# Kernel tuning notes

Measured on AMD Instinct MI355X. Metric: run time of the kernel, lower is better.

The kernel has to match this reference:

```python
import jax, jax.numpy as jnp
import numpy as np

EMBED_DIM = 256
NUM_HEADS = 8
HEAD_DIM = EMBED_DIM // NUM_HEADS
ADJ_CHANNELS = 4
B, N = 8, 1024


def setup_inputs() -> dict:
    key = jax.random.key(0)
    ks = jax.random.split(key, 12)
    s = 1.0 / np.sqrt(EMBED_DIM)
    sa = 1.0 / np.sqrt(ADJ_CHANNELS)
    return {
        "x": jax.random.normal(ks[0], (B, N, EMBED_DIM), dtype=jnp.float32),
        "adj": jax.random.uniform(ks[1], (B, N, N, ADJ_CHANNELS), dtype=jnp.float32),
        "Wq": jax.random.uniform(ks[2], (EMBED_DIM, EMBED_DIM), jnp.float32, -s, s),
        "bq": jnp.zeros((EMBED_DIM,), jnp.float32),
        "Wk": jax.random.uniform(ks[3], (EMBED_DIM, EMBED_DIM), jnp.float32, -s, s),
        "bk": jnp.zeros((EMBED_DIM,), jnp.float32),
        "Wv": jax.random.uniform(ks[4], (EMBED_DIM, EMBED_DIM), jnp.float32, -s, s),
        "bv": jnp.zeros((EMBED_DIM,), jnp.float32),
        "Wo": jax.random.uniform(ks[5], (EMBED_DIM, EMBED_DIM), jnp.float32, -s, s),
        "bo": jnp.zeros((EMBED_DIM,), jnp.float32),
        "Wa": jax.random.uniform(ks[6], (ADJ_CHANNELS, NUM_HEADS), jnp.float32, -sa, sa),
        "ba": jnp.zeros((NUM_HEADS,), jnp.float32),
    }


def reference(x, adj, Wq, bq, Wk, bk, Wv, bv, Wo, bo, Wa, ba):
    Bs, Ns, E = x.shape
    H, D = NUM_HEADS, HEAD_DIM
    def heads(W, b):
        return (x @ W + b).reshape(Bs, Ns, H, D).transpose(0, 2, 1, 3)  # [B,H,N,D]
    Q, K, V = heads(Wq, bq), heads(Wk, bk), heads(Wv, bv)
    # adjacency-derived additive bias: [B,N,N,C] -> [B,N,N,H] -> [B,H,N,N]
    bias = jnp.moveaxis(adj @ Wa + ba, -1, 1)
    scores = jnp.einsum("bhnd,bhmd->bhnm", Q, K) / np.sqrt(D) + bias
    attn = jax.nn.softmax(scores, axis=-1)
    ctx = jnp.einsum("bhnm,bhmd->bhnd", attn, V)  # [B,H,N,D]
    ctx = ctx.transpose(0, 2, 1, 3).reshape(Bs, Ns, E)
    return ctx @ Wo + bo + x
```

## Files before the change

kernel.cpp:

```cpp
#include <hip/hip_runtime.h>
#include <hip/hip_bf16.h>

#define BATCH 8
#define SEQ   1024
#define EMB   256
#define NH    8
#define HD    32
#define QSCALE 0.2550030053f

typedef __attribute__((ext_vector_type(8))) short short8;
typedef __attribute__((ext_vector_type(4))) float floatx4;

__device__ __forceinline__ ushort f2bf(float f) {
    __hip_bfloat16 h = __float2bfloat16(f);
    return *reinterpret_cast<ushort*>(&h);
}

__device__ __forceinline__ float bf2f(ushort u) {
    unsigned v = ((unsigned)u) << 16;
    return __builtin_bit_cast(float, v);
}

__device__ __forceinline__ void gload_lds16(const float4* g, float4* l) {
    __builtin_amdgcn_global_load_lds(
        (const __attribute__((address_space(1))) unsigned int*)g,
        (__attribute__((address_space(3))) unsigned int*)l, 16, 0, 0);
}

__global__ __launch_bounds__(256) void prep_kernel(
    const float* __restrict__ Wq, const float* __restrict__ Wk,
    const float* __restrict__ Wv, const float* __restrict__ Wo,
    ushort* __restrict__ Wqt, ushort* __restrict__ Wkt,
    ushort* __restrict__ Wvt, ushort* __restrict__ Wot)
{
    __shared__ float tilebuf[32][33];
    const int blk = blockIdx.x;
    const int mat = blk >> 6, tile = blk & 63;
    const int ti = tile >> 3, tj = tile & 7;
    const float* W = (mat == 0) ? Wq : (mat == 1) ? Wk : (mat == 2) ? Wv : Wo;
    ushort* Wt = (mat == 0) ? Wqt : (mat == 1) ? Wkt : (mat == 2) ? Wvt : Wot;
    const float scale = (mat == 0) ? QSCALE : 1.0f;

    const int tx = threadIdx.x & 31, ty = threadIdx.x >> 5;
    #pragma unroll
    for (int p = 0; p < 4; ++p)
        tilebuf[ty + p * 8][tx] = W[(size_t)(ti * 32 + ty + p * 8) * EMB + tj * 32 + tx];
    __syncthreads();
    #pragma unroll
    for (int p = 0; p < 4; ++p)
        Wt[(size_t)(tj * 32 + ty + p * 8) * EMB + ti * 32 + tx] =
            f2bf(tilebuf[tx][ty + p * 8] * scale);
}

__global__ __launch_bounds__(256) void qkv_gemm(
    const float* __restrict__ x,
    const ushort* __restrict__ Wqt, const ushort* __restrict__ Wkt,
    const ushort* __restrict__ Wvt,
    const float* __restrict__ bq, const float* __restrict__ bk,
    const float* __restrict__ bv,
    ushort* __restrict__ Qb, ushort* __restrict__ Kb, ushort* __restrict__ Vt)
{
    const int mat = blockIdx.y;
    const ushort* __restrict__ Wt = (mat == 0) ? Wqt : (mat == 1) ? Wkt : Wvt;
    const float* __restrict__ bias = (mat == 0) ? bq : (mat == 1) ? bk : bv;
    const float bscale = (mat == 0) ? QSCALE : 1.0f;

    const int w = threadIdx.x >> 6, lane = threadIdx.x & 63;
    const int quad = lane >> 4, l16 = lane & 15;
    const int row0 = blockIdx.x * 64 + w * 16;

    floatx4 acc[16];
    #pragma unroll
    for (int i = 0; i < 16; ++i) acc[i] = (floatx4){0.f, 0.f, 0.f, 0.f};

    const float* __restrict__ xrow = x + (size_t)(row0 + l16) * EMB + quad * 8;

    #pragma unroll
    for (int ks = 0; ks < 8; ++ks) {
        const float4 xa0 = *(const float4*)(xrow + ks * 32);
        const float4 xa1 = *(const float4*)(xrow + ks * 32 + 4);
        ushort au[8] = {f2bf(xa0.x), f2bf(xa0.y), f2bf(xa0.z), f2bf(xa0.w),
                        f2bf(xa1.x), f2bf(xa1.y), f2bf(xa1.z), f2bf(xa1.w)};
        const short8 a = *(const short8*)au;
        #pragma unroll
        for (int i = 0; i < 16; ++i) {
            const short8 bf = *(const short8*)(Wt + (size_t)(i * 16 + l16) * EMB + ks * 32 + quad * 8);
            acc[i] = __builtin_amdgcn_mfma_f32_16x16x32_bf16(a, bf, acc[i], 0, 0, 0);
        }
    }

    const int gr0 = row0 + quad * 4;
    if (mat < 2) {
        ushort* __restrict__ dst = (mat == 0) ? Qb : Kb;
        #pragma unroll
        for (int i = 0; i < 16; ++i) {
            const int c = i * 16 + l16, h = c >> 5, d = c & (HD - 1);
            const float bb = bias[c] * bscale;
            #pragma unroll
            for (int r = 0; r < 4; ++r) {
                const int gr = gr0 + r, b = gr >> 10, n = gr & (SEQ - 1);
                dst[((size_t)(b * NH + h) * SEQ + n) * HD + d] = f2bf(acc[i][r] + bb);
            }
        }
    } else {
        const int b = gr0 >> 10, n0 = gr0 & (SEQ - 1);
        const int j0 = n0 & 31;
        const int slot = (j0 < 16) ? ((j0 >> 2) << 3)
                                   : ((((j0 - 16) >> 2) << 3) + 4);
        const int nperm = (n0 & ~31) | slot;
        #pragma unroll
        for (int i = 0; i < 16; ++i) {
            const int c = i * 16 + l16, h = c >> 5, d = c & (HD - 1);
            const float bb = bias[c];
            ushort4 t4;
            t4.x = f2bf(acc[i][0] + bb); t4.y = f2bf(acc[i][1] + bb);
            t4.z = f2bf(acc[i][2] + bb); t4.w = f2bf(acc[i][3] + bb);
            *(ushort4*)(Vt + ((size_t)(b * NH + h) * HD + d) * SEQ + nperm) = t4;
        }
    }
}

__global__ __launch_bounds__(512) void attn_kernel(
    const ushort* __restrict__ Qb, const ushort* __restrict__ Kb,
    const ushort* __restrict__ Vt, const float* __restrict__ adj,
    const float* __restrict__ Wa, const float* __restrict__ ba,
    ushort* __restrict__ cp, float* __restrict__ lsum)
{
    __shared__ float4 Atile[2][16][65];
    const int tid = threadIdx.x, h = tid >> 6, lane = tid & 63;
    const int quad = lane >> 4, l16 = lane & 15;
    const int q0 = blockIdx.x * 16, b = blockIdx.y, z = blockIdx.z;
    const int bh = b * NH + h;
    const int kz = z * 512;

    const float LOG2E = 1.4426950408889634f;
    const float wa0 = Wa[0 * NH + h] * LOG2E, wa1 = Wa[1 * NH + h] * LOG2E;
    const float wa2 = Wa[2 * NH + h] * LOG2E, wa3 = Wa[3 * NH + h] * LOG2E;
    const float bah = ba[h] * LOG2E;

    const short8 aq = *(const short8*)(Qb + ((size_t)bh * SEQ + q0 + l16) * HD + quad * 8);

    floatx4 o0 = {0.f, 0.f, 0.f, 0.f}, o1 = {0.f, 0.f, 0.f, 0.f};
    float lacc = 0.f;

    const float4* __restrict__ adjb = (const float4*)adj + (size_t)b * SEQ * SEQ;
    const float4* __restrict__ asrc0 = adjb + (size_t)(q0 + 2 * h)     * SEQ + kz + lane;
    const float4* __restrict__ asrc1 = adjb + (size_t)(q0 + 2 * h + 1) * SEQ + kz + lane;

    const ushort* __restrict__ Kbase = Kb + (size_t)bh * SEQ * HD + (size_t)l16 * HD + quad * 8;
    const ushort* __restrict__ Vb0 = Vt + ((size_t)bh * HD + l16) * SEQ + quad * 8;
    const ushort* __restrict__ Vb1 = Vt + ((size_t)bh * HD + 16 + l16) * SEQ + quad * 8;

    gload_lds16(asrc0, &Atile[0][2 * h][0]);
    gload_lds16(asrc1, &Atile[0][2 * h + 1][0]);
    __syncthreads();

    for (int it = 0; it < 8; ++it) {
        const int cur = it & 1;
        const int key0 = kz + it * 64;

        if (it < 7) {
            gload_lds16(asrc0 + (it + 1) * 64, &Atile[cur ^ 1][2 * h][0]);
            gload_lds16(asrc1 + (it + 1) * 64, &Atile[cur ^ 1][2 * h + 1][0]);
        }

        const short8 k0 = *(const short8*)(Kbase + (size_t)(key0)      * HD);
        const short8 k1 = *(const short8*)(Kbase + (size_t)(key0 + 16) * HD);
        const short8 k2 = *(const short8*)(Kbase + (size_t)(key0 + 32) * HD);
        const short8 k3 = *(const short8*)(Kbase + (size_t)(key0 + 48) * HD);
        const floatx4 zz = {0.f, 0.f, 0.f, 0.f};
        floatx4 s0 = __builtin_amdgcn_mfma_f32_16x16x32_bf16(k0, aq, zz, 0, 0, 0);
        floatx4 s1 = __builtin_amdgcn_mfma_f32_16x16x32_bf16(k1, aq, zz, 0, 0, 0);
        floatx4 s2 = __builtin_amdgcn_mfma_f32_16x16x32_bf16(k2, aq, zz, 0, 0, 0);
        floatx4 s3 = __builtin_amdgcn_mfma_f32_16x16x32_bf16(k3, aq, zz, 0, 0, 0);

        ushort pu0[8], pu1[8];
        #pragma unroll
        for (int r = 0; r < 4; ++r) {
            const int col = 4 * quad + r;
            const float4 a0 = Atile[cur][l16][col];
            const float4 a1 = Atile[cur][l16][16 + col];
            const float4 a2 = Atile[cur][l16][32 + col];
            const float4 a3 = Atile[cur][l16][48 + col];
            const float b0 = fmaf(a0.x, wa0, fmaf(a0.y, wa1, fmaf(a0.z, wa2, fmaf(a0.w, wa3, bah))));
            const float b1 = fmaf(a1.x, wa0, fmaf(a1.y, wa1, fmaf(a1.z, wa2, fmaf(a1.w, wa3, bah))));
            const float b2 = fmaf(a2.x, wa0, fmaf(a2.y, wa1, fmaf(a2.z, wa2, fmaf(a2.w, wa3, bah))));
            const float b3 = fmaf(a3.x, wa0, fmaf(a3.y, wa1, fmaf(a3.z, wa2, fmaf(a3.w, wa3, bah))));
            const float p0 = __builtin_amdgcn_exp2f(s0[r] + b0);
            const float p1 = __builtin_amdgcn_exp2f(s1[r] + b1);
            const float p2 = __builtin_amdgcn_exp2f(s2[r] + b2);
            const float p3 = __builtin_amdgcn_exp2f(s3[r] + b3);
            lacc += (p0 + p1) + (p2 + p3);
            pu0[r]     = f2bf(p0);
            pu0[4 + r] = f2bf(p1);
            pu1[r]     = f2bf(p2);
            pu1[4 + r] = f2bf(p3);
        }
        const short8 pf0 = *(const short8*)pu0;
        const short8 pf1 = *(const short8*)pu1;

        const short8 v00 = *(const short8*)(Vb0 + key0);
        const short8 v10 = *(const short8*)(Vb1 + key0);
        const short8 v01 = *(const short8*)(Vb0 + key0 + 32);
        const short8 v11 = *(const short8*)(Vb1 + key0 + 32);
        o0 = __builtin_amdgcn_mfma_f32_16x16x32_bf16(v00, pf0, o0, 0, 0, 0);
        o1 = __builtin_amdgcn_mfma_f32_16x16x32_bf16(v10, pf0, o1, 0, 0, 0);
        o0 = __builtin_amdgcn_mfma_f32_16x16x32_bf16(v01, pf1, o0, 0, 0, 0);
        o1 = __builtin_amdgcn_mfma_f32_16x16x32_bf16(v11, pf1, o1, 0, 0, 0);

        __syncthreads();
    }

    lacc += __shfl_xor(lacc, 16, 64);
    lacc += __shfl_xor(lacc, 32, 64);

    ushort* __restrict__ cpz = cp + (size_t)z * BATCH * SEQ * EMB;
    float* __restrict__ lsz = lsum + (size_t)z * BATCH * SEQ * NH;
    const size_t grow = (size_t)b * SEQ + q0 + l16;
    ushort4 t0, t1;
    t0.x = f2bf(o0[0]); t0.y = f2bf(o0[1]); t0.z = f2bf(o0[2]); t0.w = f2bf(o0[3]);
    t1.x = f2bf(o1[0]); t1.y = f2bf(o1[1]); t1.z = f2bf(o1[2]); t1.w = f2bf(o1[3]);
    *(ushort4*)(cpz + grow * EMB + h * HD + 4 * quad)      = t0;
    *(ushort4*)(cpz + grow * EMB + h * HD + 16 + 4 * quad) = t1;
    if (quad == 0) lsz[grow * NH + h] = lacc;
}

__global__ __launch_bounds__(256) void outproj_gemm(
    const ushort* __restrict__ cp, const float* __restrict__ lsum,
    const ushort* __restrict__ Wot, const float* __restrict__ bo,
    const float* __restrict__ x, float* __restrict__ out)
{
    const int w = threadIdx.x >> 6, lane = threadIdx.x & 63;
    const int quad = lane >> 4, l16 = lane & 15;
    const int row0 = blockIdx.x * 64 + w * 16;
    const int c0 = blockIdx.y * 128;
    const int arow = row0 + l16;
    const ushort* __restrict__ cp1 = cp + (size_t)BATCH * SEQ * EMB;
    const float* __restrict__ l1  = lsum + (size_t)BATCH * SEQ * NH;

    floatx4 acc[8];
    #pragma unroll
    for (int i = 0; i < 8; ++i) acc[i] = (floatx4){0.f, 0.f, 0.f, 0.f};

    #pragma unroll
    for (int ks = 0; ks < 8; ++ks) {
        const float invl = 1.0f / (lsum[(size_t)arow * NH + ks] + l1[(size_t)arow * NH + ks]);
        const size_t cb = (size_t)arow * EMB + ks * 32 + quad * 8;
        const ushort4 c00 = *(const ushort4*)(cp + cb);
        const ushort4 c01 = *(const ushort4*)(cp + cb + 4);
        const ushort4 c10 = *(const ushort4*)(cp1 + cb);
        const ushort4 c11 = *(const ushort4*)(cp1 + cb + 4);
        ushort au[8] = {
            f2bf((bf2f(c00.x) + bf2f(c10.x)) * invl),
            f2bf((bf2f(c00.y) + bf2f(c10.y)) * invl),
            f2bf((bf2f(c00.z) + bf2f(c10.z)) * invl),
            f2bf((bf2f(c00.w) + bf2f(c10.w)) * invl),
            f2bf((bf2f(c01.x) + bf2f(c11.x)) * invl),
            f2bf((bf2f(c01.y) + bf2f(c11.y)) * invl),
            f2bf((bf2f(c01.z) + bf2f(c11.z)) * invl),
            f2bf((bf2f(c01.w) + bf2f(c11.w)) * invl)};
        const short8 a = *(const short8*)au;
        #pragma unroll
        for (int i = 0; i < 8; ++i) {
            const short8 bfr = *(const short8*)(Wot + (size_t)(c0 + i * 16 + l16) * EMB + ks * 32 + quad * 8);
            acc[i] = __builtin_amdgcn_mfma_f32_16x16x32_bf16(a, bfr, acc[i], 0, 0, 0);
        }
    }

    const int gr0 = row0 + quad * 4;
    #pragma unroll
    for (int i = 0; i < 8; ++i) {
        const int c = c0 + i * 16 + l16;
        const float bov = bo[c];
        #pragma unroll
        for (int r = 0; r < 4; ++r) {
            const size_t idx = (size_t)(gr0 + r) * EMB + c;
            out[idx] = acc[i][r] + bov + x[idx];
        }
    }
}

extern "C" void kernel_launch(void* const* d_in, const int* in_sizes, int n_in,
                              void* d_out, int out_size, void* d_ws, size_t ws_size,
                              hipStream_t stream) {
    const float* x   = (const float*)d_in[0];
    const float* adj = (const float*)d_in[1];
    const float* Wq  = (const float*)d_in[2];
    const float* bq  = (const float*)d_in[3];
    const float* Wk  = (const float*)d_in[4];
    const float* bk  = (const float*)d_in[5];
    const float* Wv  = (const float*)d_in[6];
    const float* bv  = (const float*)d_in[7];
    const float* Wo  = (const float*)d_in[8];
    const float* bo  = (const float*)d_in[9];
    const float* Wa  = (const float*)d_in[10];
    const float* ba  = (const float*)d_in[11];

    const size_t per = (size_t)BATCH * NH * SEQ * HD;
    ushort* Qb  = (ushort*)d_ws;
    ushort* Kb  = Qb + per;
    ushort* Vt  = Kb + per;
    ushort* Wqt = Vt + per;
    ushort* Wkt = Wqt + EMB * EMB;
    ushort* Wvt = Wkt + EMB * EMB;
    ushort* Wot = Wvt + EMB * EMB;
    ushort* cpw = Wot + EMB * EMB;
    float*  ls  = (float*)(cpw + 2 * (size_t)BATCH * SEQ * EMB);

    prep_kernel<<<256, 256, 0, stream>>>(Wq, Wk, Wv, Wo, Wqt, Wkt, Wvt, Wot);
    qkv_gemm<<<dim3(BATCH * SEQ / 64, 3), 256, 0, stream>>>(
        x, Wqt, Wkt, Wvt, bq, bk, bv, Qb, Kb, Vt);
    attn_kernel<<<dim3(SEQ / 16, BATCH, 2), 512, 0, stream>>>(
        Qb, Kb, Vt, adj, Wa, ba, cpw, ls);
    outproj_gemm<<<dim3(BATCH * SEQ / 64, 2), 256, 0, stream>>>(
        cpw, ls, Wot, bo, x, (float*)d_out);
}
```

Baseline: 299.2 us.

## Process two heads per wavefront in attention kernel to reuse adjacency LDS reads

Halves the attention block to 256 threads, with each wavefront now handling two heads instead of one. Each adjacency float4 read from LDS now feeds the bias computation for both heads, halving LDS read traffic per head. Each wave loads four adjacency rows per iteration instead of two. The cost is higher register pressure (doubled accumulators, K/V fragments and scores) and fewer waves per block, which may lower occupancy and latency hiding.

```diff
diff --git a/kernel.cpp b/kernel.cpp
--- a/kernel.cpp
+++ b/kernel.cpp
@@ -120,39 +120,51 @@
     }
 }
 
-__global__ __launch_bounds__(512) void attn_kernel(
+__global__ __launch_bounds__(256) void attn_kernel(
     const ushort* __restrict__ Qb, const ushort* __restrict__ Kb,
     const ushort* __restrict__ Vt, const float* __restrict__ adj,
     const float* __restrict__ Wa, const float* __restrict__ ba,
     ushort* __restrict__ cp, float* __restrict__ lsum)
 {
     __shared__ float4 Atile[2][16][65];
-    const int tid = threadIdx.x, h = tid >> 6, lane = tid & 63;
+    const int tid = threadIdx.x, w = tid >> 6, lane = tid & 63;
     const int quad = lane >> 4, l16 = lane & 15;
+    const int h0 = 2 * w, h1 = 2 * w + 1;
     const int q0 = blockIdx.x * 16, b = blockIdx.y, z = blockIdx.z;
-    const int bh = b * NH + h;
+    const int bh0 = b * NH + h0, bh1 = b * NH + h1;
     const int kz = z * 512;
 
     const float LOG2E = 1.4426950408889634f;
-    const float wa0 = Wa[0 * NH + h] * LOG2E, wa1 = Wa[1 * NH + h] * LOG2E;
-    const float wa2 = Wa[2 * NH + h] * LOG2E, wa3 = Wa[3 * NH + h] * LOG2E;
-    const float bah = ba[h] * LOG2E;
-
-    const short8 aq = *(const short8*)(Qb + ((size_t)bh * SEQ + q0 + l16) * HD + quad * 8);
-
-    floatx4 o0 = {0.f, 0.f, 0.f, 0.f}, o1 = {0.f, 0.f, 0.f, 0.f};
-    float lacc = 0.f;
+    const float wa00 = Wa[0 * NH + h0] * LOG2E, wa01 = Wa[1 * NH + h0] * LOG2E;
+    const float wa02 = Wa[2 * NH + h0] * LOG2E, wa03 = Wa[3 * NH + h0] * LOG2E;
+    const float bah0 = ba[h0] * LOG2E;
+    const float wa10 = Wa[0 * NH + h1] * LOG2E, wa11 = Wa[1 * NH + h1] * LOG2E;
+    const float wa12 = Wa[2 * NH + h1] * LOG2E, wa13 = Wa[3 * NH + h1] * LOG2E;
+    const float bah1 = ba[h1] * LOG2E;
+
+    const short8 aq0 = *(const short8*)(Qb + ((size_t)bh0 * SEQ + q0 + l16) * HD + quad * 8);
+    const short8 aq1 = *(const short8*)(Qb + ((size_t)bh1 * SEQ + q0 + l16) * HD + quad * 8);
+
+    floatx4 o00 = {0.f, 0.f, 0.f, 0.f}, o01 = {0.f, 0.f, 0.f, 0.f};
+    floatx4 o10 = {0.f, 0.f, 0.f, 0.f}, o11 = {0.f, 0.f, 0.f, 0.f};
+    float lacc0 = 0.f, lacc1 = 0.f;
 
     const float4* __restrict__ adjb = (const float4*)adj + (size_t)b * SEQ * SEQ;
-    const float4* __restrict__ asrc0 = adjb + (size_t)(q0 + 2 * h)     * SEQ + kz + lane;
-    const float4* __restrict__ asrc1 = adjb + (size_t)(q0 + 2 * h + 1) * SEQ + kz + lane;
-
-    const ushort* __restrict__ Kbase = Kb + (size_t)bh * SEQ * HD + (size_t)l16 * HD + quad * 8;
-    const ushort* __restrict__ Vb0 = Vt + ((size_t)bh * HD + l16) * SEQ + quad * 8;
-    const ushort* __restrict__ Vb1 = Vt + ((size_t)bh * HD + 16 + l16) * SEQ + quad * 8;
-
-    gload_lds16(asrc0, &Atile[0][2 * h][0]);
-    gload_lds16(asrc1, &Atile[0][2 * h + 1][0]);
+    const float4* asrc[4];
+    #pragma unroll
+    for (int p = 0; p < 4; ++p)
+        asrc[p] = adjb + (size_t)(q0 + 4 * w + p) * SEQ + kz + lane;
+
+    const ushort* __restrict__ Kb0 = Kb + (size_t)bh0 * SEQ * HD + (size_t)l16 * HD + quad * 8;
+    const ushort* __restrict__ Kb1 = Kb + (size_t)bh1 * SEQ * HD + (size_t)l16 * HD + quad * 8;
+    const ushort* __restrict__ Vb00 = Vt + ((size_t)bh0 * HD + l16) * SEQ + quad * 8;
+    const ushort* __restrict__ Vb01 = Vt + ((size_t)bh0 * HD + 16 + l16) * SEQ + quad * 8;
+    const ushort* __restrict__ Vb10 = Vt + ((size_t)bh1 * HD + l16) * SEQ + quad * 8;
+    const ushort* __restrict__ Vb11 = Vt + ((size_t)bh1 * HD + 16 + l16) * SEQ + quad * 8;
+
+    #pragma unroll
+    for (int p = 0; p < 4; ++p)
+        gload_lds16(asrc[p], &Atile[0][4 * w + p][0]);
     __syncthreads();
 
     for (int it = 0; it < 8; ++it) {
@@ -160,21 +172,30 @@
         const int key0 = kz + it * 64;
 
         if (it < 7) {
-            gload_lds16(asrc0 + (it + 1) * 64, &Atile[cur ^ 1][2 * h][0]);
-            gload_lds16(asrc1 + (it + 1) * 64, &Atile[cur ^ 1][2 * h + 1][0]);
-        }
-
-        const short8 k0 = *(const short8*)(Kbase + (size_t)(key0)      * HD);
-        const short8 k1 = *(const short8*)(Kbase + (size_t)(key0 + 16) * HD);
-        const short8 k2 = *(const short8*)(Kbase + (size_t)(key0 + 32) * HD);
-        const short8 k3 = *(const short8*)(Kbase + (size_t)(key0 + 48) * HD);
+            #pragma unroll
+            for (int p = 0; p < 4; ++p)
+                gload_lds16(asrc[p] + (it + 1) * 64, &Atile[cur ^ 1][4 * w + p][0]);
+        }
+
+        const short8 k00 = *(const short8*)(Kb0 + (size_t)(key0)      * HD);
+        const short8 k01 = *(const short8*)(Kb0 + (size_t)(key0 + 16) * HD);
+        const short8 k02 = *(const short8*)(Kb0 + (size_t)(key0 + 32) * HD);
+        const short8 k03 = *(const short8*)(Kb0 + (size_t)(key0 + 48) * HD);
+        const short8 k10 = *(const short8*)(Kb1 + (size_t)(key0)      * HD);
+        const short8 k11 = *(const short8*)(Kb1 + (size_t)(key0 + 16) * HD);
+        const short8 k12 = *(const short8*)(Kb1 + (size_t)(key0 + 32) * HD);
+        const short8 k13 = *(const short8*)(Kb1 + (size_t)(key0 + 48) * HD);
         const floatx4 zz = {0.f, 0.f, 0.f, 0.f};
-        floatx4 s0 = __builtin_amdgcn_mfma_f32_16x16x32_bf16(k0, aq, zz, 0, 0, 0);
-        floatx4 s1 = __builtin_amdgcn_mfma_f32_16x16x32_bf16(k1, aq, zz, 0, 0, 0);
-        floatx4 s2 = __builtin_amdgcn_mfma_f32_16x16x32_bf16(k2, aq, zz, 0, 0, 0);
-        floatx4 s3 = __builtin_amdgcn_mfma_f32_16x16x32_bf16(k3, aq, zz, 0, 0, 0);
-
-        ushort pu0[8], pu1[8];
+        floatx4 s00 = __builtin_amdgcn_mfma_f32_16x16x32_bf16(k00, aq0, zz, 0, 0, 0);
+        floatx4 s01 = __builtin_amdgcn_mfma_f32_16x16x32_bf16(k01, aq0, zz, 0, 0, 0);
+        floatx4 s02 = __builtin_amdgcn_mfma_f32_16x16x32_bf16(k02, aq0, zz, 0, 0, 0);
+        floatx4 s03 = __builtin_amdgcn_mfma_f32_16x16x32_bf16(k03, aq0, zz, 0, 0, 0);
+        floatx4 s10 = __builtin_amdgcn_mfma_f32_16x16x32_bf16(k10, aq1, zz, 0, 0, 0);
+        floatx4 s11 = __builtin_amdgcn_mfma_f32_16x16x32_bf16(k11, aq1, zz, 0, 0, 0);
+        floatx4 s12 = __builtin_amdgcn_mfma_f32_16x16x32_bf16(k12, aq1, zz, 0, 0, 0);
+        floatx4 s13 = __builtin_amdgcn_mfma_f32_16x16x32_bf16(k13, aq1, zz, 0, 0, 0);
+
+        ushort pu00[8], pu01[8], pu10[8], pu11[8];
         #pragma unroll
         for (int r = 0; r < 4; ++r) {
             const int col = 4 * quad + r;
@@ -182,47 +203,79 @@
             const float4 a1 = Atile[cur][l16][16 + col];
             const float4 a2 = Atile[cur][l16][32 + col];
             const float4 a3 = Atile[cur][l16][48 + col];
-            const float b0 = fmaf(a0.x, wa0, fmaf(a0.y, wa1, fmaf(a0.z, wa2, fmaf(a0.w, wa3, bah))));
-            const float b1 = fmaf(a1.x, wa0, fmaf(a1.y, wa1, fmaf(a1.z, wa2, fmaf(a1.w, wa3, bah))));
-            const float b2 = fmaf(a2.x, wa0, fmaf(a2.y, wa1, fmaf(a2.z, wa2, fmaf(a2.w, wa3, bah))));
-            const float b3 = fmaf(a3.x, wa0, fmaf(a3.y, wa1, fmaf(a3.z, wa2, fmaf(a3.w, wa3, bah))));
-            const float p0 = __builtin_amdgcn_exp2f(s0[r] + b0);
-            const float p1 = __builtin_amdgcn_exp2f(s1[r] + b1);
-            const float p2 = __builtin_amdgcn_exp2f(s2[r] + b2);
-            const float p3 = __builtin_amdgcn_exp2f(s3[r] + b3);
-            lacc += (p0 + p1) + (p2 + p3);
-            pu0[r]     = f2bf(p0);
-            pu0[4 + r] = f2bf(p1);
-            pu1[r]     = f2bf(p2);
-            pu1[4 + r] = f2bf(p3);
-        }
-        const short8 pf0 = *(const short8*)pu0;
-        const short8 pf1 = *(const short8*)pu1;
-
-        const short8 v00 = *(const short8*)(Vb0 + key0);
-        const short8 v10 = *(const short8*)(Vb1 + key0);
-        const short8 v01 = *(const short8*)(Vb0 + key0 + 32);
-        const short8 v11 = *(const short8*)(Vb1 + key0 + 32);
-        o0 = __builtin_amdgcn_mfma_f32_16x16x32_bf16(v00, pf0, o0, 0, 0, 0);
-        o1 = __builtin_amdgcn_mfma_f32_16x16x32_bf16(v10, pf0, o1, 0, 0, 0);
-        o0 = __builtin_amdgcn_mfma_f32_16x16x32_bf16(v01, pf1, o0, 0, 0, 0);
-        o1 = __builtin_amdgcn_mfma_f32_16x16x32_bf16(v11, pf1, o1, 0, 0, 0);
+            {
+                const float b0 = fmaf(a0.x, wa00, fmaf(a0.y, wa01, fmaf(a0.z, wa02, fmaf(a0.w, wa03, bah0))));
+                const float b1 = fmaf(a1.x, wa00, fmaf(a1.y, wa01, fmaf(a1.z, wa02, fmaf(a1.w, wa03, bah0))));
+                const float b2 = fmaf(a2.x, wa00, fmaf(a2.y, wa01, fmaf(a2.z, wa02, fmaf(a2.w, wa03, bah0))));
+                const float b3 = fmaf(a3.x, wa00, fmaf(a3.y, wa01, fmaf(a3.z, wa02, fmaf(a3.w, wa03, bah0))));
+                const float p0 = __builtin_amdgcn_exp2f(s00[r] + b0);
+                const float p1 = __builtin_amdgcn_exp2f(s01[r] + b1);
+                const float p2 = __builtin_amdgcn_exp2f(s02[r] + b2);
+                const float p3 = __builtin_amdgcn_exp2f(s03[r] + b3);
+                lacc0 += (p0 + p1) + (p2 + p3);
+                pu00[r] = f2bf(p0); pu00[4 + r] = f2bf(p1);
+                pu01[r] = f2bf(p2); pu01[4 + r] = f2bf(p3);
+            }
+            {
+                const float b0 = fmaf(a0.x, wa10, fmaf(a0.y, wa11, fmaf(a0.z, wa12, fmaf(a0.w, wa13, bah1))));
+                const float b1 = fmaf(a1.x, wa10, fmaf(a1.y, wa11, fmaf(a1.z, wa12, fmaf(a1.w, wa13, bah1))));
+                const float b2 = fmaf(a2.x, wa10, fmaf(a2.y, wa11, fmaf(a2.z, wa12, fmaf(a2.w, wa13, bah1))));
+                const float b3 = fmaf(a3.x, wa10, fmaf(a3.y, wa11, fmaf(a3.z, wa12, fmaf(a3.w, wa13, bah1))));
+                const float p0 = __builtin_amdgcn_exp2f(s10[r] + b0);
+                const float p1 = __builtin_amdgcn_exp2f(s11[r] + b1);
+                const float p2 = __builtin_amdgcn_exp2f(s12[r] + b2);
+                const float p3 = __builtin_amdgcn_exp2f(s13[r] + b3);
+                lacc1 += (p0 + p1) + (p2 + p3);
+                pu10[r] = f2bf(p0); pu10[4 + r] = f2bf(p1);
+                pu11[r] = f2bf(p2); pu11[4 + r] = f2bf(p3);
+            }
+        }
+        const short8 pf00 = *(const short8*)pu00;
+        const short8 pf01 = *(const short8*)pu01;
+        const short8 pf10 = *(const short8*)pu10;
+        const short8 pf11 = *(const short8*)pu11;
+
+        const short8 v000 = *(const short8*)(Vb00 + key0);
+        const short8 v010 = *(const short8*)(Vb01 + key0);
+        const short8 v001 = *(const short8*)(Vb00 + key0 + 32);
+        const short8 v011 = *(const short8*)(Vb01 + key0 + 32);
+        o00 = __builtin_amdgcn_mfma_f32_16x16x32_bf16(v000, pf00, o00, 0, 0, 0);
+        o01 = __builtin_amdgcn_mfma_f32_16x16x32_bf16(v010, pf00, o01, 0, 0, 0);
+        o00 = __builtin_amdgcn_mfma_f32_16x16x32_bf16(v001, pf01, o00, 0, 0, 0);
+        o01 = __builtin_amdgcn_mfma_f32_16x16x32_bf16(v011, pf01, o01, 0, 0, 0);
+        const short8 v100 = *(const short8*)(Vb10 + key0);
+        const short8 v110 = *(const short8*)(Vb11 + key0);
+        const short8 v101 = *(const short8*)(Vb10 + key0 + 32);
+        const short8 v111 = *(const short8*)(Vb11 + key0 + 32);
+        o10 = __builtin_amdgcn_mfma_f32_16x16x32_bf16(v100, pf10, o10, 0, 0, 0);
+        o11 = __builtin_amdgcn_mfma_f32_16x16x32_bf16(v110, pf10, o11, 0, 0, 0);
+        o10 = __builtin_amdgcn_mfma_f32_16x16x32_bf16(v101, pf11, o10, 0, 0, 0);
+        o11 = __builtin_amdgcn_mfma_f32_16x16x32_bf16(v111, pf11, o11, 0, 0, 0);
 
         __syncthreads();
     }
 
-    lacc += __shfl_xor(lacc, 16, 64);
-    lacc += __shfl_xor(lacc, 32, 64);
+    lacc0 += __shfl_xor(lacc0, 16, 64);
+    lacc0 += __shfl_xor(lacc0, 32, 64);
+    lacc1 += __shfl_xor(lacc1, 16, 64);
+    lacc1 += __shfl_xor(lacc1, 32, 64);
 
     ushort* __restrict__ cpz = cp + (size_t)z * BATCH * SEQ * EMB;
     float* __restrict__ lsz = lsum + (size_t)z * BATCH * SEQ * NH;
     const size_t grow = (size_t)b * SEQ + q0 + l16;
-    ushort4 t0, t1;
-    t0.x = f2bf(o0[0]); t0.y = f2bf(o0[1]); t0.z = f2bf(o0[2]); t0.w = f2bf(o0[3]);
-    t1.x = f2bf(o1[0]); t1.y = f2bf(o1[1]); t1.z = f2bf(o1[2]); t1.w = f2bf(o1[3]);
-    *(ushort4*)(cpz + grow * EMB + h * HD + 4 * quad)      = t0;
-    *(ushort4*)(cpz + grow * EMB + h * HD + 16 + 4 * quad) = t1;
-    if (quad == 0) lsz[grow * NH + h] = lacc;
+    ushort4 t;
+    t.x = f2bf(o00[0]); t.y = f2bf(o00[1]); t.z = f2bf(o00[2]); t.w = f2bf(o00[3]);
+    *(ushort4*)(cpz + grow * EMB + h0 * HD + 4 * quad)      = t;
+    t.x = f2bf(o01[0]); t.y = f2bf(o01[1]); t.z = f2bf(o01[2]); t.w = f2bf(o01[3]);
+    *(ushort4*)(cpz + grow * EMB + h0 * HD + 16 + 4 * quad) = t;
+    t.x = f2bf(o10[0]); t.y = f2bf(o10[1]); t.z = f2bf(o10[2]); t.w = f2bf(o10[3]);
+    *(ushort4*)(cpz + grow * EMB + h1 * HD + 4 * quad)      = t;
+    t.x = f2bf(o11[0]); t.y = f2bf(o11[1]); t.z = f2bf(o11[2]); t.w = f2bf(o11[3]);
+    *(ushort4*)(cpz + grow * EMB + h1 * HD + 16 + 4 * quad) = t;
+    if (quad == 0) {
+        lsz[grow * NH + h0] = lacc0;
+        lsz[grow * NH + h1] = lacc1;
+    }
 }
 
 __global__ __launch_bounds__(256) void outproj_gemm(
@@ -310,7 +363,7 @@
     prep_kernel<<<256, 256, 0, stream>>>(Wq, Wk, Wv, Wo, Wqt, Wkt, Wvt, Wot);
     qkv_gemm<<<dim3(BATCH * SEQ / 64, 3), 256, 0, stream>>>(
         x, Wqt, Wkt, Wvt, bq, bk, bv, Qb, Kb, Vt);
-    attn_kernel<<<dim3(SEQ / 16, BATCH, 2), 512, 0, stream>>>(
+    attn_kernel<<<dim3(SEQ / 16, BATCH, 2), 256, 0, stream>>>(
         Qb, Kb, Vt, adj, Wa, ba, cpw, ls);
     outproj_gemm<<<dim3(BATCH * SEQ / 64, 2), 256, 0, stream>>>(
         cpw, ls, Wot, bo, x, (float*)d_out);
```

New measurement: 307.8 us. 2.9% more time.
